# Kernel optimization log

Hardware: AMD Instinct MI355X
Metric: run time of the kernel (lower is better)

## Reference

```python
import jax, jax.numpy as jnp
import numpy as np

N_NODES = 100000
N_EDGES = 1600000
IN_DIM, FEAT_DIM, HID_DIM, OUT_DIM = 256, 128, 128, 128


def _glorot(key, shape):
    lim = float(np.sqrt(6.0 / (shape[0] + shape[1])))
    return jax.random.uniform(key, shape, jnp.float32, -lim, lim)


def setup_inputs() -> dict:
    key = jax.random.key(0)
    ks = jax.random.split(key, 6)
    x = jax.random.normal(ks[0], (N_NODES, IN_DIM), jnp.float32)
    edge_index = jax.random.randint(ks[1], (2, N_EDGES), 0, N_NODES, dtype=jnp.int64)
    return {
        "x": x,
        "edge_index": edge_index,
        "Wp": _glorot(ks[2], (IN_DIM, FEAT_DIM)),
        "bp": jnp.zeros((FEAT_DIM,), jnp.float32),
        "W1": _glorot(ks[3], (FEAT_DIM, HID_DIM)),
        "b1": jnp.zeros((HID_DIM,), jnp.float32),
        "W2": _glorot(ks[4], (HID_DIM, OUT_DIM)),
        "b2": jnp.zeros((OUT_DIM,), jnp.float32),
    }


def _gcn_conv(h, W, b, src, dst, norm, deg_inv, n):
    # PyG GCNConv: linear first, symmetric-normalized aggregation (with
    # self-loops), bias after aggregation. Self-loop term = z_i / deg_i.
    z = h @ W                                   # [N, out]
    msg = (norm[src] * norm[dst])[:, None] * z[src]  # [E, out]
    agg = jax.ops.segment_sum(msg, dst, num_segments=n)
    return agg + z * deg_inv[:, None] + b


def reference(x, edge_index, Wp, bp, W1, b1, W2, b2):
    src, dst = edge_index[0], edge_index[1]
    n = x.shape[0]
    # degrees on A + I (self-loop adds 1)
    deg = jax.ops.segment_sum(jnp.ones(src.shape[0], x.dtype), dst, num_segments=n) + 1.0
    norm = jax.lax.rsqrt(deg)
    deg_inv = 1.0 / deg
    h = x @ Wp + bp                              # feature_pre linear
    h = jax.nn.relu(_gcn_conv(h, W1, b1, src, dst, norm, deg_inv, n))
    # dropout is identity in eval mode; layer_num=2 -> no hidden convs
    return _gcn_conv(h, W2, b2, src, dst, norm, deg_inv, n)
```

## Files before the change

### kernel.cpp

```cpp
#include <hip/hip_runtime.h>
#include <cstdint>
#include <cstddef>

#define N_NODES 100000
#define N_EDGES 1600000

constexpr int NPB = 512;
constexpr int NBUCK = (N_NODES + NPB - 1) / NPB;
constexpr int EPB = 8192;
constexpr int NCHUNK = (N_EDGES + EPB - 1) / EPB;

typedef _Float16 half8 __attribute__((ext_vector_type(8)));
typedef _Float16 half2v __attribute__((ext_vector_type(2)));
typedef float f32x4 __attribute__((ext_vector_type(4)));

__global__ __launch_bounds__(256) void b1_hist(const int* __restrict__ dst,
                                               int* __restrict__ bbc) {
    __shared__ int hist[NBUCK];
    int t = threadIdx.x;
    if (t < NBUCK) hist[t] = 0;
    __syncthreads();
    int base = blockIdx.x * EPB;
#pragma unroll
    for (int i = 0; i < EPB / 256; ++i) {
        int e = base + i * 256 + t;
        if (e < N_EDGES) atomicAdd(&hist[dst[e] >> 9], 1);
    }
    __syncthreads();
    if (t < NBUCK) bbc[t * NCHUNK + blockIdx.x] = hist[t];
}

__global__ void b_scan(int* __restrict__ bbc, int* __restrict__ bucketOff,
                       int* __restrict__ rowStart) {
    __shared__ int tot[NBUCK];
    int t = threadIdx.x;
    if (t < NBUCK) {
        int run = 0;
        for (int blk = 0; blk < NCHUNK; ++blk) {
            int idx = t * NCHUNK + blk;
            int c = bbc[idx];
            bbc[idx] = run;
            run += c;
        }
        tot[t] = run;
    }
    __syncthreads();
    if (t == 0) {
        int acc = 0;
        for (int b = 0; b < NBUCK; ++b) {
            bucketOff[b] = acc;
            acc += tot[b];
        }
        bucketOff[NBUCK] = acc;
        rowStart[N_NODES] = acc;
    }
}

__global__ __launch_bounds__(256) void b2_scatter(const int* __restrict__ src,
                                                  const int* __restrict__ dst,
                                                  const int* __restrict__ bbc,
                                                  const int* __restrict__ bucketOff,
                                                  int* __restrict__ staged) {
    __shared__ int cnt[NBUCK];
    __shared__ int base[NBUCK];
    int t = threadIdx.x;
    if (t < NBUCK) {
        cnt[t] = 0;
        base[t] = bucketOff[t] + bbc[t * NCHUNK + blockIdx.x];
    }
    __syncthreads();
    int ebase = blockIdx.x * EPB;
#pragma unroll
    for (int i = 0; i < EPB / 256; ++i) {
        int e = ebase + i * 256 + t;
        if (e < N_EDGES) {
            int d = dst[e];
            int b = d >> 9;
            int r = atomicAdd(&cnt[b], 1);
            staged[base[b] + r] = ((d & 511) << 17) | src[e];
        }
    }
}

__global__ __launch_bounds__(256) void b3_sort(const int* __restrict__ staged,
                                               const int* __restrict__ bucketOff,
                                               int* __restrict__ rowStart,
                                               float* __restrict__ normv,
                                               int* __restrict__ colIdx) {
    __shared__ int hist[NPB];
    __shared__ int sc0[NPB], sc1[NPB];
    __shared__ int cursor[NPB];
    int t = threadIdx.x;
    int b = blockIdx.x;
    int e0 = bucketOff[b], e1 = bucketOff[b + 1];
    int ne = e1 - e0;
    int node0 = b * NPB;
    int nn = min(NPB, N_NODES - node0);

    for (int j = t; j < NPB; j += 256) hist[j] = 0;
    __syncthreads();
    for (int idx = t; idx < ne; idx += 256)
        atomicAdd(&hist[staged[e0 + idx] >> 17], 1);
    __syncthreads();
    for (int j = t; j < NPB; j += 256) sc0[j] = hist[j];
    __syncthreads();
    int* s = sc0;
    int* d = sc1;
    for (int off = 1; off < NPB; off <<= 1) {
        for (int j = t; j < NPB; j += 256) d[j] = s[j] + (j >= off ? s[j - off] : 0);
        __syncthreads();
        int* tmp = s; s = d; d = tmp;
    }
    for (int j = t; j < NPB; j += 256) {
        int excl = s[j] - hist[j];
        cursor[j] = excl;
        if (j < nn) {
            rowStart[node0 + j] = e0 + excl;
            normv[node0 + j] = (float)(1.0 / sqrt((double)(hist[j] + 1)));
        }
    }
    __syncthreads();
    for (int idx = t; idx < ne; idx += 256) {
        int v = staged[e0 + idx];
        int dl = v >> 17;
        int sn = v & 0x1FFFF;
        int r = atomicAdd(&cursor[dl], 1);
        colIdx[e0 + r] = sn;
    }
}

__global__ void wc_kernel(const float* __restrict__ Wp, const float* __restrict__ bp,
                          const float* __restrict__ W1, float* __restrict__ Wc,
                          float* __restrict__ bc) {
    int r = blockIdx.x;
    int cc = threadIdx.x;
    float acc = 0.f;
    if (r < 256) {
        for (int k = 0; k < 128; ++k) acc = fmaf(Wp[r * 128 + k], W1[k * 128 + cc], acc);
        Wc[r * 128 + cc] = acc;
    } else {
        for (int k = 0; k < 128; ++k) acc = fmaf(bp[k], W1[k * 128 + cc], acc);
        bc[cc] = acc;
    }
}

__global__ void tsplit_kernel(const float* __restrict__ W, _Float16* __restrict__ Oh,
                              _Float16* __restrict__ Ol, int K) {
    int id = blockIdx.x * 256 + threadIdx.x;
    if (id >= K * 128) return;
    int n = id / K;
    int k = id - n * K;
    float v = W[k * 128 + n];
    _Float16 h = (_Float16)v;
    Oh[id] = h;
    Ol[id] = (_Float16)(v - (float)h);
}

template <bool AF16>
__global__ __launch_bounds__(256) void mfma_gemm(const float* __restrict__ Af,
                                                 const _Float16* __restrict__ Ah,
                                                 const _Float16* __restrict__ Bth,
                                                 const _Float16* __restrict__ Btl,
                                                 const float* __restrict__ bias,
                                                 const float* __restrict__ scale,
                                                 float* __restrict__ Cf,
                                                 _Float16* __restrict__ Ch,
                                                 int M, int K) {
    const int t = threadIdx.x;
    const int w = t >> 6;
    const int lane = t & 63;
    const int q = lane >> 4;
    const int mr = lane & 15;
    const int row0 = blockIdx.x * 128 + w * 32;

    int ar0 = row0 + mr;        if (ar0 >= M) ar0 = 0;
    int ar1 = row0 + 16 + mr;   if (ar1 >= M) ar1 = 0;

    f32x4 acc[2][8];
#pragma unroll
    for (int mt = 0; mt < 2; ++mt)
#pragma unroll
        for (int nt = 0; nt < 8; ++nt) acc[mt][nt] = (f32x4){0.f, 0.f, 0.f, 0.f};

    for (int k0 = 0; k0 < K; k0 += 32) {
        const int kf = k0 + q * 8;
        half8 ah[2], al[2];
        if constexpr (AF16) {
            ah[0] = *(const half8*)(Ah + (size_t)ar0 * K + kf);
            ah[1] = *(const half8*)(Ah + (size_t)ar1 * K + kf);
        } else {
#pragma unroll
            for (int mt = 0; mt < 2; ++mt) {
                int row = mt ? ar1 : ar0;
                const float* ap = Af + (size_t)row * K + kf;
                float4 v0 = *(const float4*)ap;
                float4 v1 = *(const float4*)(ap + 4);
                float av[8] = {v0.x, v0.y, v0.z, v0.w, v1.x, v1.y, v1.z, v1.w};
#pragma unroll
                for (int j = 0; j < 8; ++j) {
                    _Float16 h = (_Float16)av[j];
                    ah[mt][j] = h;
                    al[mt][j] = (_Float16)(av[j] - (float)h);
                }
            }
        }
#pragma unroll
        for (int nt = 0; nt < 8; ++nt) {
            int n = nt * 16 + mr;
            half8 bh = *(const half8*)(Bth + (size_t)n * K + kf);
            half8 bl = *(const half8*)(Btl + (size_t)n * K + kf);
#pragma unroll
            for (int mt = 0; mt < 2; ++mt) {
                acc[mt][nt] = __builtin_amdgcn_mfma_f32_16x16x32_f16(ah[mt], bh, acc[mt][nt], 0, 0, 0);
                acc[mt][nt] = __builtin_amdgcn_mfma_f32_16x16x32_f16(ah[mt], bl, acc[mt][nt], 0, 0, 0);
                if constexpr (!AF16)
                    acc[mt][nt] = __builtin_amdgcn_mfma_f32_16x16x32_f16(al[mt], bh, acc[mt][nt], 0, 0, 0);
            }
        }
    }

#pragma unroll
    for (int mt = 0; mt < 2; ++mt) {
#pragma unroll
        for (int r = 0; r < 4; ++r) {
            int row = row0 + mt * 16 + q * 4 + r;
            if (row >= M) continue;
            float sc = scale[row];
#pragma unroll
            for (int nt = 0; nt < 8; ++nt) {
                int col = nt * 16 + mr;
                float bv = bias ? bias[col] : 0.f;
                float val = (acc[mt][nt][r] + bv) * sc;
                if (Ch) Ch[(size_t)row * 128 + col] = (_Float16)val;
                else    Cf[(size_t)row * 128 + col] = val;
            }
        }
    }
}

__global__ __launch_bounds__(256) void agg_kernel(const _Float16* __restrict__ zs,
                                                  const int* __restrict__ rowStart,
                                                  const int* __restrict__ colIdx,
                                                  const float* __restrict__ normv,
                                                  const float* __restrict__ bias,
                                                  float* __restrict__ outF,
                                                  _Float16* __restrict__ outH,
                                                  int doRelu) {
    int wid = (blockIdx.x * 256 + threadIdx.x) >> 6;
    int lane = threadIdx.x & 63;
    if (wid >= N_NODES) return;
    int s0 = rowStart[wid];
    int s1 = rowStart[wid + 1];
    const int c = lane * 2;
    const _Float16* zc = zs + c;

    float2 a0 = make_float2(0.f, 0.f), a1 = a0, a2 = a0, a3 = a0;
    int e = s0;
    for (; e + 8 <= s1; e += 8) {
        int i0 = colIdx[e + 0], i1 = colIdx[e + 1], i2 = colIdx[e + 2], i3 = colIdx[e + 3];
        int i4 = colIdx[e + 4], i5 = colIdx[e + 5], i6 = colIdx[e + 6], i7 = colIdx[e + 7];
        half2v v0 = *(const half2v*)(zc + (size_t)i0 * 128);
        half2v v1 = *(const half2v*)(zc + (size_t)i1 * 128);
        half2v v2 = *(const half2v*)(zc + (size_t)i2 * 128);
        half2v v3 = *(const half2v*)(zc + (size_t)i3 * 128);
        half2v v4 = *(const half2v*)(zc + (size_t)i4 * 128);
        half2v v5 = *(const half2v*)(zc + (size_t)i5 * 128);
        half2v v6 = *(const half2v*)(zc + (size_t)i6 * 128);
        half2v v7 = *(const half2v*)(zc + (size_t)i7 * 128);
        a0.x += (float)v0[0] + (float)v4[0]; a0.y += (float)v0[1] + (float)v4[1];
        a1.x += (float)v1[0] + (float)v5[0]; a1.y += (float)v1[1] + (float)v5[1];
        a2.x += (float)v2[0] + (float)v6[0]; a2.y += (float)v2[1] + (float)v6[1];
        a3.x += (float)v3[0] + (float)v7[0]; a3.y += (float)v3[1] + (float)v7[1];
    }
    if (e + 4 <= s1) {
        int i0 = colIdx[e + 0], i1 = colIdx[e + 1], i2 = colIdx[e + 2], i3 = colIdx[e + 3];
        half2v v0 = *(const half2v*)(zc + (size_t)i0 * 128);
        half2v v1 = *(const half2v*)(zc + (size_t)i1 * 128);
        half2v v2 = *(const half2v*)(zc + (size_t)i2 * 128);
        half2v v3 = *(const half2v*)(zc + (size_t)i3 * 128);
        a0.x += (float)v0[0]; a0.y += (float)v0[1];
        a1.x += (float)v1[0]; a1.y += (float)v1[1];
        a2.x += (float)v2[0]; a2.y += (float)v2[1];
        a3.x += (float)v3[0]; a3.y += (float)v3[1];
        e += 4;
    }
    for (; e < s1; ++e) {
        int i0 = colIdx[e];
        half2v v0 = *(const half2v*)(zc + (size_t)i0 * 128);
        a0.x += (float)v0[0]; a0.y += (float)v0[1];
    }

    half2v self = *(const half2v*)(zc + (size_t)wid * 128);
    float sx = (a0.x + a1.x) + (a2.x + a3.x) + (float)self[0];
    float sy = (a0.y + a1.y) + (a2.y + a3.y) + (float)self[1];
    float nd = normv[wid];
    float2 bv = *(const float2*)(bias + c);
    float ox = fmaf(nd, sx, bv.x);
    float oy = fmaf(nd, sy, bv.y);
    if (doRelu) {
        ox = fmaxf(ox, 0.f);
        oy = fmaxf(oy, 0.f);
    }
    if (outH) {
        half2v o;
        o[0] = (_Float16)ox;
        o[1] = (_Float16)oy;
        *(half2v*)(outH + (size_t)wid * 128 + c) = o;
    } else {
        *(float2*)(outF + (size_t)wid * 128 + c) = make_float2(ox, oy);
    }
}

extern "C" void kernel_launch(void* const* d_in, const int* in_sizes, int n_in,
                              void* d_out, int out_size, void* d_ws, size_t ws_size,
                              hipStream_t stream) {
    const float* x  = (const float*)d_in[0];
    const int* ei   = (const int*)d_in[1];
    const float* Wp = (const float*)d_in[2];
    const float* bp = (const float*)d_in[3];
    const float* W1 = (const float*)d_in[4];
    const float* b1 = (const float*)d_in[5];
    const float* W2 = (const float*)d_in[6];
    const float* b2 = (const float*)d_in[7];
    float* out = (float*)d_out;

    const int* srcIdx = ei;
    const int* dstIdx = ei + N_EDGES;

    size_t off = 0;
    auto alloc = [&](size_t bytes) -> void* {
        void* p = (char*)d_ws + off;
        off += (bytes + 511) & ~(size_t)511;
        return p;
    };
    int* rowStart   = (int*)alloc((size_t)(N_NODES + 1) * 4);
    int* colIdx     = (int*)alloc((size_t)N_EDGES * 4);
    int* staged     = (int*)alloc((size_t)N_EDGES * 4);
    int* bbc        = (int*)alloc((size_t)NBUCK * NCHUNK * 4);
    int* bucketOff  = (int*)alloc((size_t)(NBUCK + 1) * 4);
    float* normv    = (float*)alloc((size_t)N_NODES * 4);
    float* Wc       = (float*)alloc((size_t)256 * 128 * 4);
    float* bc       = (float*)alloc((size_t)128 * 4);
    _Float16* Wcth  = (_Float16*)alloc((size_t)128 * 256 * 2);
    _Float16* Wctl  = (_Float16*)alloc((size_t)128 * 256 * 2);
    _Float16* W2th  = (_Float16*)alloc((size_t)128 * 128 * 2);
    _Float16* W2tl  = (_Float16*)alloc((size_t)128 * 128 * 2);
    _Float16* zA    = (_Float16*)alloc((size_t)N_NODES * 128 * 2);
    _Float16* zB    = (_Float16*)alloc((size_t)N_NODES * 128 * 2);

    const int GB = (N_NODES + 127) / 128;
    const int AB = (N_NODES + 3) / 4;

    b1_hist<<<NCHUNK, 256, 0, stream>>>(dstIdx, bbc);
    b_scan<<<1, 256, 0, stream>>>(bbc, bucketOff, rowStart);
    b2_scatter<<<NCHUNK, 256, 0, stream>>>(srcIdx, dstIdx, bbc, bucketOff, staged);
    b3_sort<<<NBUCK, 256, 0, stream>>>(staged, bucketOff, rowStart, normv, colIdx);

    wc_kernel<<<257, 128, 0, stream>>>(Wp, bp, W1, Wc, bc);
    tsplit_kernel<<<(256 * 128 + 255) / 256, 256, 0, stream>>>(Wc, Wcth, Wctl, 256);
    tsplit_kernel<<<(128 * 128 + 255) / 256, 256, 0, stream>>>(W2, W2th, W2tl, 128);

    mfma_gemm<false><<<GB, 256, 0, stream>>>(x, nullptr, Wcth, Wctl, bc, normv,
                                             nullptr, zA, N_NODES, 256);
    agg_kernel<<<AB, 256, 0, stream>>>(zA, rowStart, colIdx, normv, b1, nullptr, zB, 1);
    mfma_gemm<true><<<GB, 256, 0, stream>>>(nullptr, zB, W2th, W2tl, nullptr, normv,
                                            nullptr, zA, N_NODES, 128);
    agg_kernel<<<AB, 256, 0, stream>>>(zA, rowStart, colIdx, normv, b2, out, nullptr, 0);
}
```

Measured before the change: 516.5 us.

## Stage GEMM B tiles in double-buffered LDS with 2x2 wave tiling and A prefetch

The MFMA GEMM now loads the split-fp16 weight slabs cooperatively into double-buffered shared memory instead of each wave reading them from global memory. The four waves form a 2x2 grid of 64x64 sub-tiles, which raises B reuse. The next slab's A and B values are prefetched into registers during the current MFMAs. K becomes a template parameter so the loop is fully unrolled, at the cost of more registers and LDS and a sync per slab.

```diff
diff --git a/kernel.cpp b/kernel.cpp
--- a/kernel.cpp
+++ b/kernel.cpp
@@ -156,7 +156,7 @@
     Ol[id] = (_Float16)(v - (float)h);
 }
 
-template <bool AF16>
+template <bool AF16, int K>
 __global__ __launch_bounds__(256) void mfma_gemm(const float* __restrict__ Af,
                                                  const _Float16* __restrict__ Ah,
                                                  const _Float16* __restrict__ Bth,
@@ -165,37 +165,77 @@
                                                  const float* __restrict__ scale,
                                                  float* __restrict__ Cf,
                                                  _Float16* __restrict__ Ch,
-                                                 int M, int K) {
+                                                 int M) {
+    constexpr int NSLAB = K / 32;
+    __shared__ _Float16 sBh[2][128 * 40];
+    __shared__ _Float16 sBl[2][128 * 40];
+
     const int t = threadIdx.x;
     const int w = t >> 6;
+    const int wm = w & 1;
+    const int wn = w >> 1;
     const int lane = t & 63;
     const int q = lane >> 4;
     const int mr = lane & 15;
-    const int row0 = blockIdx.x * 128 + w * 32;
-
-    int ar0 = row0 + mr;        if (ar0 >= M) ar0 = 0;
-    int ar1 = row0 + 16 + mr;   if (ar1 >= M) ar1 = 0;
-
-    f32x4 acc[2][8];
-#pragma unroll
-    for (int mt = 0; mt < 2; ++mt)
-#pragma unroll
-        for (int nt = 0; nt < 8; ++nt) acc[mt][nt] = (f32x4){0.f, 0.f, 0.f, 0.f};
-
-    for (int k0 = 0; k0 < K; k0 += 32) {
-        const int kf = k0 + q * 8;
-        half8 ah[2], al[2];
+    const int row0 = blockIdx.x * 128 + wm * 64;
+    const int col0 = wn * 64;
+
+    const int sn = t >> 1;
+    const int sseg = t & 1;
+    const _Float16* gBh = Bth + (size_t)sn * K + sseg * 16;
+    const _Float16* gBl = Btl + (size_t)sn * K + sseg * 16;
+    const int swoff = sn * 40 + sseg * 16;
+
+    int arow[4];
+#pragma unroll
+    for (int mt = 0; mt < 4; ++mt) {
+        int r = row0 + mt * 16 + mr;
+        arow[mt] = (r < M) ? r : (M - 1);
+    }
+
+    f32x4 acc[4][4];
+#pragma unroll
+    for (int mt = 0; mt < 4; ++mt)
+#pragma unroll
+        for (int nt = 0; nt < 4; ++nt) acc[mt][nt] = (f32x4){0.f, 0.f, 0.f, 0.f};
+
+    {
+        half8 h0 = *(const half8*)(gBh);
+        half8 h1 = *(const half8*)(gBh + 8);
+        half8 l0 = *(const half8*)(gBl);
+        half8 l1 = *(const half8*)(gBl + 8);
+        *(half8*)&sBh[0][swoff] = h0;
+        *(half8*)&sBh[0][swoff + 8] = h1;
+        *(half8*)&sBl[0][swoff] = l0;
+        *(half8*)&sBl[0][swoff + 8] = l1;
+    }
+    float4 aPre0[4], aPre1[4];
+    half8  aPreH[4];
+#pragma unroll
+    for (int mt = 0; mt < 4; ++mt) {
         if constexpr (AF16) {
-            ah[0] = *(const half8*)(Ah + (size_t)ar0 * K + kf);
-            ah[1] = *(const half8*)(Ah + (size_t)ar1 * K + kf);
+            aPreH[mt] = *(const half8*)(Ah + (size_t)arow[mt] * K + q * 8);
         } else {
-#pragma unroll
-            for (int mt = 0; mt < 2; ++mt) {
-                int row = mt ? ar1 : ar0;
-                const float* ap = Af + (size_t)row * K + kf;
-                float4 v0 = *(const float4*)ap;
-                float4 v1 = *(const float4*)(ap + 4);
-                float av[8] = {v0.x, v0.y, v0.z, v0.w, v1.x, v1.y, v1.z, v1.w};
+            const float* ap = Af + (size_t)arow[mt] * K + q * 8;
+            aPre0[mt] = *(const float4*)ap;
+            aPre1[mt] = *(const float4*)(ap + 4);
+        }
+    }
+    __syncthreads();
+
+#pragma unroll
+    for (int s = 0; s < NSLAB; ++s) {
+        const int cur = s & 1;
+        const int nxt = 1 - cur;
+
+        half8 ah[4], al[4];
+#pragma unroll
+        for (int mt = 0; mt < 4; ++mt) {
+            if constexpr (AF16) {
+                ah[mt] = aPreH[mt];
+            } else {
+                float av[8] = {aPre0[mt].x, aPre0[mt].y, aPre0[mt].z, aPre0[mt].w,
+                               aPre1[mt].x, aPre1[mt].y, aPre1[mt].z, aPre1[mt].w};
 #pragma unroll
                 for (int j = 0; j < 8; ++j) {
                     _Float16 h = (_Float16)av[j];
@@ -204,31 +244,63 @@
                 }
             }
         }
-#pragma unroll
-        for (int nt = 0; nt < 8; ++nt) {
-            int n = nt * 16 + mr;
-            half8 bh = *(const half8*)(Bth + (size_t)n * K + kf);
-            half8 bl = *(const half8*)(Btl + (size_t)n * K + kf);
-#pragma unroll
-            for (int mt = 0; mt < 2; ++mt) {
-                acc[mt][nt] = __builtin_amdgcn_mfma_f32_16x16x32_f16(ah[mt], bh, acc[mt][nt], 0, 0, 0);
-                acc[mt][nt] = __builtin_amdgcn_mfma_f32_16x16x32_f16(ah[mt], bl, acc[mt][nt], 0, 0, 0);
+
+        half8 nh0, nh1, nl0, nl1;
+        if (s + 1 < NSLAB) {
+            const int ko = (s + 1) * 32;
+            nh0 = *(const half8*)(gBh + ko);
+            nh1 = *(const half8*)(gBh + ko + 8);
+            nl0 = *(const half8*)(gBl + ko);
+            nl1 = *(const half8*)(gBl + ko + 8);
+#pragma unroll
+            for (int mt = 0; mt < 4; ++mt) {
+                if constexpr (AF16) {
+                    aPreH[mt] = *(const half8*)(Ah + (size_t)arow[mt] * K + ko + q * 8);
+                } else {
+                    const float* ap = Af + (size_t)arow[mt] * K + ko + q * 8;
+                    aPre0[mt] = *(const float4*)ap;
+                    aPre1[mt] = *(const float4*)(ap + 4);
+                }
+            }
+        }
+
+        half8 bh[4], bl[4];
+#pragma unroll
+        for (int nt = 0; nt < 4; ++nt) {
+            int n = col0 + nt * 16 + mr;
+            bh[nt] = *(half8*)&sBh[cur][n * 40 + q * 8];
+            bl[nt] = *(half8*)&sBl[cur][n * 40 + q * 8];
+        }
+
+#pragma unroll
+        for (int mt = 0; mt < 4; ++mt)
+#pragma unroll
+            for (int nt = 0; nt < 4; ++nt) {
+                acc[mt][nt] = __builtin_amdgcn_mfma_f32_16x16x32_f16(ah[mt], bh[nt], acc[mt][nt], 0, 0, 0);
+                acc[mt][nt] = __builtin_amdgcn_mfma_f32_16x16x32_f16(ah[mt], bl[nt], acc[mt][nt], 0, 0, 0);
                 if constexpr (!AF16)
-                    acc[mt][nt] = __builtin_amdgcn_mfma_f32_16x16x32_f16(al[mt], bh, acc[mt][nt], 0, 0, 0);
+                    acc[mt][nt] = __builtin_amdgcn_mfma_f32_16x16x32_f16(al[mt], bh[nt], acc[mt][nt], 0, 0, 0);
             }
-        }
-    }
-
-#pragma unroll
-    for (int mt = 0; mt < 2; ++mt) {
+
+        if (s + 1 < NSLAB) {
+            *(half8*)&sBh[nxt][swoff] = nh0;
+            *(half8*)&sBh[nxt][swoff + 8] = nh1;
+            *(half8*)&sBl[nxt][swoff] = nl0;
+            *(half8*)&sBl[nxt][swoff + 8] = nl1;
+            __syncthreads();
+        }
+    }
+
+#pragma unroll
+    for (int mt = 0; mt < 4; ++mt) {
 #pragma unroll
         for (int r = 0; r < 4; ++r) {
             int row = row0 + mt * 16 + q * 4 + r;
             if (row >= M) continue;
             float sc = scale[row];
 #pragma unroll
-            for (int nt = 0; nt < 8; ++nt) {
-                int col = nt * 16 + mr;
+            for (int nt = 0; nt < 4; ++nt) {
+                int col = col0 + nt * 16 + mr;
                 float bv = bias ? bias[col] : 0.f;
                 float val = (acc[mt][nt][r] + bv) * sc;
                 if (Ch) Ch[(size_t)row * 128 + col] = (_Float16)val;
@@ -360,10 +432,10 @@
     tsplit_kernel<<<(256 * 128 + 255) / 256, 256, 0, stream>>>(Wc, Wcth, Wctl, 256);
     tsplit_kernel<<<(128 * 128 + 255) / 256, 256, 0, stream>>>(W2, W2th, W2tl, 128);
 
-    mfma_gemm<false><<<GB, 256, 0, stream>>>(x, nullptr, Wcth, Wctl, bc, normv,
-                                             nullptr, zA, N_NODES, 256);
+    mfma_gemm<false, 256><<<GB, 256, 0, stream>>>(x, nullptr, Wcth, Wctl, bc, normv,
+                                                  nullptr, zA, N_NODES);
     agg_kernel<<<AB, 256, 0, stream>>>(zA, rowStart, colIdx, normv, b1, nullptr, zB, 1);
-    mfma_gemm<true><<<GB, 256, 0, stream>>>(nullptr, zB, W2th, W2tl, nullptr, normv,
-                                            nullptr, zA, N_NODES, 128);
+    mfma_gemm<true, 128><<<GB, 256, 0, stream>>>(nullptr, zB, W2th, W2tl, nullptr, normv,
+                                                 nullptr, zA, N_NODES);
     agg_kernel<<<AB, 256, 0, stream>>>(zA, rowStart, colIdx, normv, b2, out, nullptr, 0);
 }
```

After: 477.2 us. 1.08x faster.
